# Kernel tuning notes

Hardware: AMD Instinct MI355X
Metric: run time of the kernel (lower is better)

Reference implementation:

```python
import jax, jax.numpy as jnp
import numpy as np

N_NODES = 50000
N_EDGES = 800000
H = 128
CHEM_DIM = 34   # 2 + 2*num_gdf
GEOM_DIM = 48   # 2*num_gdf + num_signatures
EPS = 1e-5


def _linear_params(key, d_in, d_out):
    kw, kb = jax.random.split(key)
    lim = 1.0 / np.sqrt(d_in)
    w = jax.random.uniform(kw, (d_in, d_out), jnp.float32, -lim, lim)
    b = jax.random.uniform(kb, (d_out,), jnp.float32, -lim, lim)
    return w, b


def setup_inputs() -> dict:
    key = jax.random.key(0)
    ks = jax.random.split(key, 16)
    inp = {
        'chem_feats': jax.random.normal(ks[0], (N_EDGES, CHEM_DIM), jnp.float32),
        'geom_feats': jax.random.normal(ks[1], (N_NODES, GEOM_DIM), jnp.float32),
        'nbr_vids': jax.random.randint(ks[2], (N_EDGES,), 0, N_NODES, jnp.int32),
    }
    # chem_mlp: Linear(34,128) -> BN(128) -> SiLU -> Linear(128,256) -> BN(256)
    inp['w_c1'], inp['b_c1'] = _linear_params(ks[3], CHEM_DIM, H)
    inp['g_c1'], inp['be_c1'] = jnp.ones((H,), jnp.float32), jnp.zeros((H,), jnp.float32)
    inp['w_c2'], inp['b_c2'] = _linear_params(ks[4], H, 2 * H)
    inp['g_c2'], inp['be_c2'] = jnp.ones((2 * H,), jnp.float32), jnp.zeros((2 * H,), jnp.float32)
    # geom_mlp: Linear(48,64) -> BN(64) -> SiLU -> Linear(64,64) -> BN(64)
    inp['w_g1'], inp['b_g1'] = _linear_params(ks[5], GEOM_DIM, H // 2)
    inp['g_g1'], inp['be_g1'] = jnp.ones((H // 2,), jnp.float32), jnp.zeros((H // 2,), jnp.float32)
    inp['w_g2'], inp['b_g2'] = _linear_params(ks[6], H // 2, H // 2)
    inp['g_g2'], inp['be_g2'] = jnp.ones((H // 2,), jnp.float32), jnp.zeros((H // 2,), jnp.float32)
    # feat_mlp: Linear(192,128) -> BN(128) -> SiLU -> Linear(128,128) -> BN(128)
    inp['w_f1'], inp['b_f1'] = _linear_params(ks[7], H + H // 2, H)
    inp['g_f1'], inp['be_f1'] = jnp.ones((H,), jnp.float32), jnp.zeros((H,), jnp.float32)
    inp['w_f2'], inp['b_f2'] = _linear_params(ks[8], H, H)
    inp['g_f2'], inp['be_f2'] = jnp.ones((H,), jnp.float32), jnp.zeros((H,), jnp.float32)
    return inp


def _bn(x, gamma, beta):
    # BatchNorm1d with batch statistics (training-mode normalization; dropout = identity at eval)
    m = jnp.mean(x, axis=0)
    v = jnp.var(x, axis=0)
    return gamma * (x - m) * jax.lax.rsqrt(v + EPS) + beta


def reference(chem_feats, geom_feats, nbr_vids,
              w_c1, b_c1, g_c1, be_c1, w_c2, b_c2, g_c2, be_c2,
              w_g1, b_g1, g_g1, be_g1, w_g2, b_g2, g_g2, be_g2,
              w_f1, b_f1, g_f1, be_f1, w_f2, b_f2, g_f2, be_f2):
    # chem branch: per-edge MLP
    h = _bn(chem_feats @ w_c1 + b_c1, g_c1, be_c1)
    h = jax.nn.silu(h)
    h = _bn(h @ w_c2 + b_c2, g_c2, be_c2)            # [E, 2H]
    nbr_filter, nbr_core = jnp.split(h, 2, axis=-1)
    h_chem = jax.nn.sigmoid(nbr_filter) * jax.nn.softplus(nbr_core)  # [E, H]
    # scatter-sum per-edge features into node bins
    h_chem = jax.ops.segment_sum(h_chem, nbr_vids, num_segments=N_NODES)  # [N, H]
    # geom branch: per-node MLP
    hg = _bn(geom_feats @ w_g1 + b_g1, g_g1, be_g1)
    hg = jax.nn.silu(hg)
    h_geom = _bn(hg @ w_g2 + b_g2, g_g2, be_g2)      # [N, H/2]
    # fuse
    hf = jnp.concatenate((h_chem, h_geom), axis=-1)  # [N, 3H/2]
    hf = _bn(hf @ w_f1 + b_f1, g_f1, be_f1)
    hf = jax.nn.silu(hf)
    h_out = _bn(hf @ w_f2 + b_f2, g_f2, be_f2)       # [N, H]
    return h_out
```

## Files before the change

### kernel.cpp

```cpp
#include <hip/hip_runtime.h>
#include <hip/hip_bf16.h>
#include <cmath>

#define E_EDGES 800000
#define N_NODES 50000
#define BN_EPS 1e-5f

typedef __attribute__((ext_vector_type(8))) short short8;
typedef __attribute__((ext_vector_type(4))) float float4v;
typedef __attribute__((ext_vector_type(4))) unsigned int uint4v;
typedef unsigned short ushort_t;

#define MFMA16(a, b, c) __builtin_amdgcn_mfma_f32_16x16x32_bf16((a), (b), (c), 0, 0, 0)

#define OFF_GX 0
#define OFF_GH 2304
#define OFF_A1 23040
#define OFF_C1 23168
#define OFF_A2 23296
#define OFF_C2 23552
#define OFF_GS1SUM 23808
#define OFF_GS1SQ 23872
#define OFF_GS2SUM 23936
#define OFF_GS2SQ 24000
#define OFF_FS1SUM 24064
#define OFF_FS1SQ 24192
#define OFF_FS2SUM 24320
#define OFF_FS2SQ 24448
#define OFF_NODE 24576
#define OFF_TG2 (OFF_NODE + N_NODES * 128)
#define OFF_TF1 (OFF_TG2 + N_NODES * 64)
#define OFF_TF2 OFF_NODE
#define OFF_W1T (OFF_TF1 + N_NODES * 128)
#define OFF_W2T (OFF_W1T + 4096)
#define OFF_BASEI (OFF_W2T + 16384)
#define OFF_BTOT (OFF_BASEI + 50176)
#define OFF_CNT (OFF_BTOT + 256)
#define OFF_CUR (OFF_CNT + 50176)
#define OFF_SIDX (OFF_CUR + 50176)
#define OFF_VIDS (OFF_SIDX + E_EDGES)

__device__ __forceinline__ float frcp_(float x) { return __builtin_amdgcn_rcpf(x); }
__device__ __forceinline__ float sigmoid_(float x) { return frcp_(1.0f + __expf(-x)); }
__device__ __forceinline__ float softplus_(float x) {
  return (x > 20.0f) ? x : __logf(1.0f + __expf(x));
}
__device__ __forceinline__ float silu_(float x) { return x * frcp_(1.0f + __expf(-x)); }

__device__ __forceinline__ ushort_t f2bf(float f) {
  __hip_bfloat16 h = __float2bfloat16(f);
  return *(ushort_t*)&h;
}
__device__ __forceinline__ float bf2f(ushort_t u) {
  return __uint_as_float(((unsigned)u) << 16);
}
__device__ __forceinline__ unsigned cvtpk(float lo, float hi) {
  unsigned r;
  asm("v_cvt_pk_bf16_f32 %0, %1, %2" : "=v"(r) : "v"(lo), "v"(hi));
  return r;
}

__device__ __forceinline__ void load_xfrag(const float* __restrict__ chem, int e, int qd,
                                           short8* x0, short8* x1) {
  const float* xe = chem + e * 34;
  float2 p0 = *(const float2*)(xe + 8 * qd);
  float2 p1 = *(const float2*)(xe + 8 * qd + 2);
  float2 p2 = *(const float2*)(xe + 8 * qd + 4);
  float2 p3 = *(const float2*)(xe + 8 * qd + 6);
  union { short8 s; uint4v u; } cv;
  cv.u[0] = cvtpk(p0.x, p0.y);
  cv.u[1] = cvtpk(p1.x, p1.y);
  cv.u[2] = cvtpk(p2.x, p2.y);
  cv.u[3] = cvtpk(p3.x, p3.y);
  *x0 = cv.s;
  union { short8 s; uint4v u; } cb;
  cb.u = (uint4v){0, 0, 0, 0};
  if (qd == 0) {
    float2 pt = *(const float2*)(xe + 32);
    cb.u[0] = cvtpk(pt.x, pt.y);
  }
  *x1 = cb.s;
}

__global__ __launch_bounds__(256) void k_prep(const float* __restrict__ w1,
                                              const float* __restrict__ w2,
                                              float* __restrict__ ws) {
  ushort_t* w1t = (ushort_t*)(ws + OFF_W1T);
  ushort_t* w2t = (ushort_t*)(ws + OFF_W2T);
  int idx = blockIdx.x * 256 + threadIdx.x;
  if (idx < 128 * 64) {
    int c = idx >> 6, k = idx & 63;
    float v = (k < 34) ? w1[k * 128 + c] : 0.0f;
    w1t[idx] = f2bf(v);
  }
  int j = idx - 128 * 64;
  if (j >= 0 && j < 256 * 128) {
    int c = j >> 7, k = j & 127;
    w2t[j] = f2bf(w2[k * 256 + c]);
  }
}

__global__ __launch_bounds__(256) void k_hist(const int* __restrict__ vids,
                                              float* __restrict__ ws) {
  const int e = blockIdx.x * 256 + threadIdx.x;
  int* cnt = (int*)(ws + OFF_CNT);
  if (e < E_EDGES) atomicAdd(&cnt[vids[e]], 1);
}

__global__ __launch_bounds__(256) void k_scan1(float* __restrict__ ws) {
  const int* cnt = (const int*)(ws + OFF_CNT);
  int* base = (int*)(ws + OFF_BASEI);
  int* btot = (int*)(ws + OFF_BTOT);
  const int t = threadIdx.x, b = blockIdx.x, i = b * 256 + t;
  const int lane = t & 63, w = t >> 6;
  int c = (i < N_NODES) ? cnt[i] : 0;
  int s = c;
#pragma unroll
  for (int o = 1; o < 64; o <<= 1) {
    int y = __shfl_up(s, o);
    if (lane >= o) s += y;
  }
  __shared__ int wsum[4];
  if (lane == 63) wsum[w] = s;
  __syncthreads();
  int add = 0;
#pragma unroll
  for (int k = 0; k < 4; ++k)
    if (k < w) add += wsum[k];
  base[i] = s + add - c;
  if (t == 255) btot[b] = s + add;
}

__global__ __launch_bounds__(256) void k_scan2(float* __restrict__ ws) {
  int* btot = (int*)(ws + OFF_BTOT);
  const int t = threadIdx.x;
  const int lane = t & 63, w = t >> 6;
  int c = (t < 196) ? btot[t] : 0;
  int s = c;
#pragma unroll
  for (int o = 1; o < 64; o <<= 1) {
    int y = __shfl_up(s, o);
    if (lane >= o) s += y;
  }
  __shared__ int wsum[4];
  if (lane == 63) wsum[w] = s;
  __syncthreads();
  int add = 0;
#pragma unroll
  for (int k = 0; k < 4; ++k)
    if (k < w) add += wsum[k];
  if (t < 196) btot[t] = s + add - c;
}

__global__ __launch_bounds__(256) void k_fill(const int* __restrict__ vids,
                                              float* __restrict__ ws) {
  const int e = blockIdx.x * 256 + threadIdx.x;
  const int* base = (const int*)(ws + OFF_BASEI);
  const int* btot = (const int*)(ws + OFF_BTOT);
  int* cur = (int*)(ws + OFF_CUR);
  int* sidx = (int*)(ws + OFF_SIDX);
  int* vsrt = (int*)(ws + OFF_VIDS);
  if (e < E_EDGES) {
    int v = vids[e];
    int pos = base[v] + btot[v >> 8] + atomicAdd(&cur[v], 1);
    sidx[pos] = e;
    vsrt[pos] = v;
  }
}

__global__ __launch_bounds__(256) void k_xstats(const float* __restrict__ chem,
                                                float* __restrict__ ws) {
  __shared__ __align__(16) ushort_t xT[2][48 * 72];
  const int t = threadIdx.x, wv = t >> 6, ln = t & 63, r15 = ln & 15, qd = ln >> 4;
  for (int i = t; i < 2 * 14 * 72; i += 256) {
    int b = i / (14 * 72), j = i % (14 * 72);
    int rr = j / 72, e = j % 72;
    xT[b][(34 + rr) * 72 + e] = (rr == 0 && e < 64) ? (ushort_t)0x3F80 : (ushort_t)0;
  }
  float4v g0 = {0, 0, 0, 0}, g1 = {0, 0, 0, 0};
#pragma unroll 2
  for (int it = 0; it < 10; ++it) {
    const int st = blockIdx.x * 10 + it;
    const int buf = it & 1;
    for (int i = t; i < 64 * 17; i += 256) {
      int e = i / 17, kp = i - e * 17;
      float2 v = *(const float2*)(chem + st * 2176 + e * 34 + 2 * kp);
      unsigned u = cvtpk(v.x, v.y);
      xT[buf][(2 * kp) * 72 + e] = (ushort_t)u;
      xT[buf][(2 * kp + 1) * 72 + e] = (ushort_t)(u >> 16);
    }
    __syncthreads();
    const ushort_t* xb = &xT[buf][0];
#pragma unroll
    for (int ks = 0; ks < 2; ++ks) {
      const ushort_t* xk = xb + ks * 32 + 8 * qd;
      short8 f0 = *(const short8*)&xk[(0 + r15) * 72];
      short8 f1 = *(const short8*)&xk[(16 + r15) * 72];
      short8 f2v = *(const short8*)&xk[(32 + r15) * 72];
      if (wv == 0) { g0 = MFMA16(f0, f0, g0); g1 = MFMA16(f0, f1, g1); }
      else if (wv == 1) { g0 = MFMA16(f0, f2v, g0); g1 = MFMA16(f1, f1, g1); }
      else if (wv == 2) { g0 = MFMA16(f1, f2v, g0); }
      else { g0 = MFMA16(f2v, f2v, g0); }
    }
  }
  float* GX = ws + OFF_GX;
  int ti0, tj0, ti1 = -1, tj1 = -1;
  if (wv == 0) { ti0 = 0; tj0 = 0; ti1 = 0; tj1 = 1; }
  else if (wv == 1) { ti0 = 0; tj0 = 2; ti1 = 1; tj1 = 1; }
  else if (wv == 2) { ti0 = 1; tj0 = 2; }
  else { ti0 = 2; tj0 = 2; }
#pragma unroll
  for (int r = 0; r < 4; ++r)
    atomicAdd(&GX[(16 * ti0 + 4 * qd + r) * 48 + 16 * tj0 + r15], g0[r]);
  if (ti1 >= 0)
#pragma unroll
    for (int r = 0; r < 4; ++r)
      atomicAdd(&GX[(16 * ti1 + 4 * qd + r) * 48 + 16 * tj1 + r15], g1[r]);
}

__global__ __launch_bounds__(64) void k_bn1(const float* __restrict__ b1,
                                            const float* __restrict__ g1,
                                            const float* __restrict__ be1,
                                            float* __restrict__ ws) {
  const int c = blockIdx.x, i = threadIdx.x;
  __shared__ float wc[34];
  const ushort_t* w1t = (const ushort_t*)(ws + OFF_W1T);
  const float* GX = ws + OFF_GX;
  if (i < 34) wc[i] = bf2f(w1t[c * 64 + i]);
  __syncthreads();
  float p = 0.0f, ps = 0.0f;
  if (i < 34) {
    float gi = 0.0f;
    for (int j = 0; j < 34; ++j) {
      int a = i, b = j;
      if ((a >> 4) > (b >> 4)) { int tt = a; a = b; b = tt; }
      gi += GX[a * 48 + b] * wc[j];
    }
    p = wc[i] * gi;
    ps = wc[i] * GX[i * 48 + 34];
  }
#pragma unroll
  for (int off = 1; off < 64; off <<= 1) {
    p += __shfl_xor(p, off);
    ps += __shfl_xor(ps, off);
  }
  if (i == 0) {
    const float E = (float)E_EDGES;
    float bc = b1[c];
    float sum = ps + E * bc;
    float sq = p + 2.0f * bc * ps + E * bc * bc;
    float m = sum / E, v = sq / E - m * m;
    float a = g1[c] * rsqrtf(v + BN_EPS);
    ws[OFF_A1 + c] = a;
    ws[OFF_C1 + c] = a * (bc - m) + be1[c];
  }
}

template <int TJA, int TJB>
__device__ __forceinline__ void ghstep(const ushort_t* hk, int r15, float4v (&g)[11]) {
  short8 f[TJB + 1];
#pragma unroll
  for (int i = 0; i <= TJB; ++i) f[i] = *(const short8*)&hk[(16 * i + r15) * 72];
  short8 f8 = *(const short8*)&hk[(128 + r15) * 72];
  int s = 0;
#pragma unroll
  for (int ti = 0; ti <= TJA; ++ti) { g[s] = MFMA16(f[ti], f[TJA], g[s]); ++s; }
  g[s] = MFMA16(f8, f[TJA], g[s]); ++s;
#pragma unroll
  for (int ti = 0; ti <= TJB; ++ti) { g[s] = MFMA16(f[ti], f[TJB], g[s]); ++s; }
  g[s] = MFMA16(f8, f[TJB], g[s]);
}

__device__ __forceinline__ void ghtile(float* GH, int ti, int tj, int r15, int qd,
                                       const float4v v) {
#pragma unroll
  for (int r = 0; r < 4; ++r)
    atomicAdd(&GH[(16 * ti + 4 * qd + r) * 144 + 16 * tj + r15], v[r]);
}

template <int TJA, int TJB>
__device__ __forceinline__ void ghflush(float* GH, int r15, int qd, const float4v (&g)[11]) {
  int s = 0;
#pragma unroll
  for (int ti = 0; ti <= TJA; ++ti) { ghtile(GH, ti, TJA, r15, qd, g[s]); ++s; }
  ghtile(GH, 8, TJA, r15, qd, g[s]); ++s;
#pragma unroll
  for (int ti = 0; ti <= TJB; ++ti) { ghtile(GH, ti, TJB, r15, qd, g[s]); ++s; }
  ghtile(GH, 8, TJB, r15, qd, g[s]);
}

__global__ __launch_bounds__(256) void k_h(const float* __restrict__ chem,
                                           float* __restrict__ ws) {
  __shared__ __align__(16) ushort_t hT[2][144 * 72];
  const int t = threadIdx.x, wv = t >> 6, ln = t & 63, r15 = ln & 15, qd = ln >> 4;
  const ushort_t* w1t = (const ushort_t*)(ws + OFF_W1T);
  for (int i = t; i < 2 * 16 * 72; i += 256) {
    int b = i / (16 * 72), j = i % (16 * 72);
    int rr = j / 72, e = j % 72;
    hT[b][(128 + rr) * 72 + e] = (rr == 0 && e < 64) ? (ushort_t)0x3F80 : (ushort_t)0;
  }
  float a1c[2], c1c[2];
#pragma unroll
  for (int cf = 0; cf < 2; ++cf) {
    int col = 32 * wv + 16 * cf + r15;
    a1c[cf] = ws[OFF_A1 + col];
    c1c[cf] = ws[OFF_C1 + col];
  }
  float4v gacc[11];
#pragma unroll
  for (int s = 0; s < 11; ++s) gacc[s] = (float4v){0, 0, 0, 0};

#pragma unroll 2
  for (int it = 0; it < 10; ++it) {
    const int st = blockIdx.x * 10 + it;
    const int buf = it & 1;
    const int e_base = st * 64;
    short8 xa0[4], xa1[4];
#pragma unroll
    for (int rb = 0; rb < 4; ++rb)
      load_xfrag(chem, e_base + 16 * rb + r15, qd, &xa0[rb], &xa1[rb]);
#pragma unroll
    for (int cf = 0; cf < 2; ++cf) {
      const int col = 32 * wv + 16 * cf + r15;
      short8 wb0 = *(const short8*)&w1t[col * 64 + 8 * qd];
      short8 wb1 = *(const short8*)&w1t[col * 64 + 32 + 8 * qd];
#pragma unroll
      for (int rb = 0; rb < 4; ++rb) {
        float4v acc = (float4v){0, 0, 0, 0};
        acc = MFMA16(xa0[rb], wb0, acc);
        acc = MFMA16(xa1[rb], wb1, acc);
        float h0 = silu_(fmaf(a1c[cf], acc[0], c1c[cf]));
        float h1 = silu_(fmaf(a1c[cf], acc[1], c1c[cf]));
        float h2 = silu_(fmaf(a1c[cf], acc[2], c1c[cf]));
        float h3 = silu_(fmaf(a1c[cf], acc[3], c1c[cf]));
        unsigned lo = cvtpk(h0, h1), hi = cvtpk(h2, h3);
        unsigned long long pk = ((unsigned long long)hi << 32) | (unsigned long long)lo;
        *(unsigned long long*)&hT[buf][col * 72 + 16 * rb + 4 * qd] = pk;
      }
    }
    __syncthreads();
    const ushort_t* hb = &hT[buf][0];
#pragma unroll
    for (int ks = 0; ks < 2; ++ks) {
      const ushort_t* hk = hb + ks * 32 + 8 * qd;
      if (wv == 0) ghstep<0, 7>(hk, r15, gacc);
      else if (wv == 1) ghstep<1, 6>(hk, r15, gacc);
      else if (wv == 2) ghstep<2, 5>(hk, r15, gacc);
      else ghstep<3, 4>(hk, r15, gacc);
    }
  }
  float* GH = ws + OFF_GH;
  if (wv == 0) ghflush<0, 7>(GH, r15, qd, gacc);
  else if (wv == 1) ghflush<1, 6>(GH, r15, qd, gacc);
  else if (wv == 2) ghflush<2, 5>(GH, r15, qd, gacc);
  else ghflush<3, 4>(GH, r15, qd, gacc);
}

__global__ __launch_bounds__(128) void k_bn2(const float* __restrict__ b2,
                                             const float* __restrict__ g2,
                                             const float* __restrict__ be2,
                                             float* __restrict__ ws) {
  const int c = blockIdx.x, i = threadIdx.x;
  __shared__ float wcol[128];
  __shared__ float redQ[2], redS[2];
  const ushort_t* w2t = (const ushort_t*)(ws + OFF_W2T);
  const float* GH = ws + OFF_GH;
  wcol[i] = bf2f(w2t[c * 128 + i]);
  __syncthreads();
  float wi = wcol[i];
  float gi = 0.0f;
  for (int j = 0; j < 128; ++j) {
    int a = i, b = j;
    if ((a >> 4) > (b >> 4)) { int tt = a; a = b; b = tt; }
    gi += GH[a * 144 + b] * wcol[j];
  }
  float p = wi * gi;
  float ps = wi * GH[128 * 144 + i];
#pragma unroll
  for (int off = 1; off < 64; off <<= 1) {
    p += __shfl_xor(p, off);
    ps += __shfl_xor(ps, off);
  }
  const int wv = i >> 6, ln = i & 63;
  if (ln == 0) { redQ[wv] = p; redS[wv] = ps; }
  __syncthreads();
  if (i == 0) {
    float q = redQ[0] + redQ[1], s = redS[0] + redS[1];
    const float E = (float)E_EDGES;
    float bc = b2[c];
    float sum = s + E * bc;
    float sq = q + 2.0f * bc * s + E * bc * bc;
    float m = sum / E, v = sq / E - m * m;
    float a = g2[c] * rsqrtf(v + BN_EPS);
    ws[OFF_A2 + c] = a;
    ws[OFF_C2 + c] = a * (bc - m) + be2[c];
  }
}

__global__ __launch_bounds__(256) void k_scatter(const float* __restrict__ chem,
                                                 float* __restrict__ ws) {
  __shared__ __align__(16) ushort_t hS[64 * 136];
  __shared__ __align__(16) float gS[32 * 133];
  __shared__ int vS[64];
  const int t = threadIdx.x, wv = t >> 6, ln = t & 63, r15 = ln & 15, qd = ln >> 4;
  const ushort_t* w1t = (const ushort_t*)(ws + OFF_W1T);
  const ushort_t* w2t = (const ushort_t*)(ws + OFF_W2T);
  const int* sidx = (const int*)(ws + OFF_SIDX);
  const int* vsrt = (const int*)(ws + OFF_VIDS);
  float* node = ws + OFF_NODE;
  float a1c[2], c1c[2], aF2[2], cF2[2], aC2[2], cC2[2];
#pragma unroll
  for (int cf = 0; cf < 2; ++cf) {
    int col = 32 * wv + 16 * cf + r15;
    a1c[cf] = ws[OFF_A1 + col];
    c1c[cf] = ws[OFF_C1 + col];
    aF2[cf] = ws[OFF_A2 + col];
    cF2[cf] = ws[OFF_C2 + col];
    aC2[cf] = ws[OFF_A2 + 128 + col];
    cC2[cf] = ws[OFF_C2 + 128 + col];
  }
  const int st0 = blockIdx.x * 8;
  int eid_cur = 0, vid_cur = 0;
  if (st0 < 12500) { eid_cur = sidx[st0 * 64 + ln]; vid_cur = vsrt[st0 * 64 + ln]; }
  for (int it = 0; it < 8; ++it) {
    const int st = st0 + it;
    if (st >= 12500) break;
    int eid_nxt = 0, vid_nxt = 0;
    if (it < 7 && st + 1 < 12500) {
      eid_nxt = sidx[(st + 1) * 64 + ln];
      vid_nxt = vsrt[(st + 1) * 64 + ln];
    }
    short8 xa0[4], xa1[4];
#pragma unroll
    for (int rb = 0; rb < 4; ++rb) {
      int er = __shfl(eid_cur, 16 * rb + r15);
      load_xfrag(chem, er, qd, &xa0[rb], &xa1[rb]);
    }
#pragma unroll
    for (int cf = 0; cf < 2; ++cf) {
      const int col = 32 * wv + 16 * cf + r15;
      short8 wb0 = *(const short8*)&w1t[col * 64 + 8 * qd];
      short8 wb1 = *(const short8*)&w1t[col * 64 + 32 + 8 * qd];
#pragma unroll
      for (int rb = 0; rb < 4; ++rb) {
        float4v acc = (float4v){0, 0, 0, 0};
        acc = MFMA16(xa0[rb], wb0, acc);
        acc = MFMA16(xa1[rb], wb1, acc);
#pragma unroll
        for (int r = 0; r < 4; ++r) {
          float hv = silu_(fmaf(a1c[cf], acc[r], c1c[cf]));
          hS[(16 * rb + 4 * qd + r) * 136 + col] = (ushort_t)cvtpk(hv, hv);
        }
      }
    }
    __syncthreads();
    if (t < 64) vS[t] = vid_cur;
#pragma unroll
    for (int ch = 0; ch < 2; ++ch) {
#pragma unroll
      for (int cf = 0; cf < 2; ++cf) {
        const int colF = 32 * wv + 16 * cf + r15;
        float4v accF[2], accC[2];
#pragma unroll
        for (int rbb = 0; rbb < 2; ++rbb) {
          accF[rbb] = (float4v){0, 0, 0, 0};
          accC[rbb] = (float4v){0, 0, 0, 0};
        }
#pragma unroll
        for (int ks = 0; ks < 4; ++ks) {
          short8 bF = *(const short8*)&w2t[colF * 128 + ks * 32 + 8 * qd];
          short8 bC = *(const short8*)&w2t[(128 + colF) * 128 + ks * 32 + 8 * qd];
#pragma unroll
          for (int rbb = 0; rbb < 2; ++rbb) {
            const int rb = 2 * ch + rbb;
            short8 hf = *(const short8*)&hS[(16 * rb + r15) * 136 + ks * 32 + 8 * qd];
            accF[rbb] = MFMA16(hf, bF, accF[rbb]);
            accC[rbb] = MFMA16(hf, bC, accC[rbb]);
          }
        }
#pragma unroll
        for (int rbb = 0; rbb < 2; ++rbb)
#pragma unroll
          for (int r = 0; r < 4; ++r) {
            float F = fmaf(aF2[cf], accF[rbb][r], cF2[cf]);
            float Co = fmaf(aC2[cf], accC[rbb][r], cC2[cf]);
            gS[(16 * rbb + 4 * qd + r) * 133 + colF] = sigmoid_(F) * softplus_(Co);
          }
      }
      __syncthreads();
      {
        const int c = t & 127, sub = t >> 7;
        const float* g = &gS[(16 * sub) * 133 + c];
        const int* vv = &vS[32 * ch + 16 * sub];
        float acc = g[0];
        int vcur = vv[0];
#pragma unroll
        for (int r = 1; r < 16; ++r) {
          int v = vv[r];
          float x = g[r * 133];
          if (v != vcur) {
            atomicAdd(node + (size_t)vcur * 128 + c, acc);
            acc = 0.0f;
            vcur = v;
          }
          acc += x;
        }
        atomicAdd(node + (size_t)vcur * 128 + c, acc);
      }
      __syncthreads();
    }
    eid_cur = eid_nxt;
    vid_cur = vid_nxt;
  }
}

__global__ __launch_bounds__(256) void k_geom_stats1(const float* __restrict__ geom,
                                                     const float* __restrict__ wg1,
                                                     const float* __restrict__ bg1,
                                                     float* __restrict__ ws) {
  __shared__ float ssum[64], ssq[64];
  const int t = threadIdx.x, lane = t & 63, w = t >> 6;
  if (t < 64) { ssum[t] = 0.0f; ssq[t] = 0.0f; }
  __syncthreads();
  const float bcol = bg1[lane];
  const int nb = blockIdx.x * 16 + w * 4;
  float x[4], acc[4];
#pragma unroll
  for (int u = 0; u < 4; u++) {
    x[u] = (lane < 48) ? geom[(nb + u) * 48 + lane] : 0.0f;
    acc[u] = bcol;
  }
#pragma unroll 16
  for (int k = 0; k < 48; k++) {
    float wvv = wg1[k * 64 + lane];
#pragma unroll
    for (int u = 0; u < 4; u++) acc[u] = fmaf(__shfl(x[u], k), wvv, acc[u]);
  }
  float bs = 0.0f, bq = 0.0f;
#pragma unroll
  for (int u = 0; u < 4; u++) { bs += acc[u]; bq += acc[u] * acc[u]; }
  atomicAdd(&ssum[lane], bs);
  atomicAdd(&ssq[lane], bq);
  __syncthreads();
  if (t < 64) {
    atomicAdd(ws + OFF_GS1SUM + t, ssum[t]);
    atomicAdd(ws + OFF_GS1SQ + t, ssq[t]);
  }
}

__global__ __launch_bounds__(256) void k_geom_main(
    const float* __restrict__ geom, const float* __restrict__ wg1,
    const float* __restrict__ bg1, const float* __restrict__ gg1,
    const float* __restrict__ beg1, const float* __restrict__ wg2,
    const float* __restrict__ bg2, float* __restrict__ ws) {
  __shared__ float ssum[64], ssq[64];
  const int t = threadIdx.x, lane = t & 63, w = t >> 6;
  if (t < 64) { ssum[t] = 0.0f; ssq[t] = 0.0f; }
  const float invN = 1.0f / (float)N_NODES;
  float s1 = ws[OFF_GS1SUM + lane], q1 = ws[OFF_GS1SQ + lane];
  float m1 = s1 * invN, v1 = q1 * invN - m1 * m1;
  float a1 = gg1[lane] * rsqrtf(v1 + BN_EPS);
  float c1 = beg1[lane] - a1 * m1;
  const float bcol = bg1[lane], b2col = bg2[lane];
  __syncthreads();
  const int nb = blockIdx.x * 16 + w * 4;
  float x[4], tg1[4], hg[4], acc[4];
#pragma unroll
  for (int u = 0; u < 4; u++) {
    x[u] = (lane < 48) ? geom[(nb + u) * 48 + lane] : 0.0f;
    tg1[u] = bcol;
  }
#pragma unroll 16
  for (int k = 0; k < 48; k++) {
    float wvv = wg1[k * 64 + lane];
#pragma unroll
    for (int u = 0; u < 4; u++) tg1[u] = fmaf(__shfl(x[u], k), wvv, tg1[u]);
  }
#pragma unroll
  for (int u = 0; u < 4; u++) {
    hg[u] = silu_(fmaf(a1, tg1[u], c1));
    acc[u] = b2col;
  }
#pragma unroll 16
  for (int k = 0; k < 64; k++) {
    float wvv = wg2[k * 64 + lane];
#pragma unroll
    for (int u = 0; u < 4; u++) acc[u] = fmaf(__shfl(hg[u], k), wvv, acc[u]);
  }
  float bs = 0.0f, bq = 0.0f;
#pragma unroll
  for (int u = 0; u < 4; u++) {
    ws[OFF_TG2 + (nb + u) * 64 + lane] = acc[u];
    bs += acc[u]; bq += acc[u] * acc[u];
  }
  atomicAdd(&ssum[lane], bs);
  atomicAdd(&ssq[lane], bq);
  __syncthreads();
  if (t < 64) {
    atomicAdd(ws + OFF_GS2SUM + t, ssum[t]);
    atomicAdd(ws + OFF_GS2SQ + t, ssq[t]);
  }
}

__global__ __launch_bounds__(256) void k_fuse1(const float* __restrict__ wf1,
                                               const float* __restrict__ bf1,
                                               const float* __restrict__ gg2,
                                               const float* __restrict__ beg2,
                                               float* __restrict__ ws) {
  __shared__ float ssum[128], ssq[128];
  const int t = threadIdx.x, lane = t & 63, w = t >> 6;
  if (t < 128) { ssum[t] = 0.0f; ssq[t] = 0.0f; }
  const float invN = 1.0f / (float)N_NODES;
  float s2 = ws[OFF_GS2SUM + lane], q2 = ws[OFF_GS2SQ + lane];
  float mg = s2 * invN, vg = q2 * invN - mg * mg;
  float ag = gg2[lane] * rsqrtf(vg + BN_EPS);
  float cg_ = beg2[lane] - ag * mg;
  const float bA = bf1[lane], bB = bf1[64 + lane];
  __syncthreads();
  const int nb = blockIdx.x * 16 + w * 4;
  float xa[4], xb[4], xg[4], acc1[4], acc2[4];
#pragma unroll
  for (int u = 0; u < 4; u++) {
    int n = nb + u;
    xa[u] = ws[OFF_NODE + n * 128 + lane];
    xb[u] = ws[OFF_NODE + n * 128 + 64 + lane];
    xg[u] = fmaf(ag, ws[OFF_TG2 + n * 64 + lane], cg_);
    acc1[u] = bA; acc2[u] = bB;
  }
#pragma unroll 16
  for (int k = 0; k < 64; k++) {
    float w1v = wf1[k * 128 + lane], w2v = wf1[k * 128 + 64 + lane];
#pragma unroll
    for (int u = 0; u < 4; u++) {
      float xk = __shfl(xa[u], k);
      acc1[u] = fmaf(xk, w1v, acc1[u]);
      acc2[u] = fmaf(xk, w2v, acc2[u]);
    }
  }
#pragma unroll 16
  for (int k = 0; k < 64; k++) {
    float w1v = wf1[(64 + k) * 128 + lane], w2v = wf1[(64 + k) * 128 + 64 + lane];
#pragma unroll
    for (int u = 0; u < 4; u++) {
      float xk = __shfl(xb[u], k);
      acc1[u] = fmaf(xk, w1v, acc1[u]);
      acc2[u] = fmaf(xk, w2v, acc2[u]);
    }
  }
#pragma unroll 16
  for (int k = 0; k < 64; k++) {
    float w1v = wf1[(128 + k) * 128 + lane], w2v = wf1[(128 + k) * 128 + 64 + lane];
#pragma unroll
    for (int u = 0; u < 4; u++) {
      float xk = __shfl(xg[u], k);
      acc1[u] = fmaf(xk, w1v, acc1[u]);
      acc2[u] = fmaf(xk, w2v, acc2[u]);
    }
  }
  float sA = 0, qA = 0, sB = 0, qB = 0;
#pragma unroll
  for (int u = 0; u < 4; u++) {
    int n = nb + u;
    ws[OFF_TF1 + n * 128 + lane] = acc1[u];
    ws[OFF_TF1 + n * 128 + 64 + lane] = acc2[u];
    sA += acc1[u]; qA += acc1[u] * acc1[u];
    sB += acc2[u]; qB += acc2[u] * acc2[u];
  }
  atomicAdd(&ssum[lane], sA); atomicAdd(&ssq[lane], qA);
  atomicAdd(&ssum[64 + lane], sB); atomicAdd(&ssq[64 + lane], qB);
  __syncthreads();
  if (t < 128) {
    atomicAdd(ws + OFF_FS1SUM + t, ssum[t]);
    atomicAdd(ws + OFF_FS1SQ + t, ssq[t]);
  }
}

__global__ __launch_bounds__(256) void k_fuse2(const float* __restrict__ wf2,
                                               const float* __restrict__ bf2,
                                               const float* __restrict__ gf1,
                                               const float* __restrict__ bef1,
                                               float* __restrict__ ws) {
  __shared__ float ssum[128], ssq[128];
  const int t = threadIdx.x, lane = t & 63, w = t >> 6;
  if (t < 128) { ssum[t] = 0.0f; ssq[t] = 0.0f; }
  const float invN = 1.0f / (float)N_NODES;
  float sA_ = ws[OFF_FS1SUM + lane], qA_ = ws[OFF_FS1SQ + lane];
  float mA = sA_ * invN, vA = qA_ * invN - mA * mA;
  float aA = gf1[lane] * rsqrtf(vA + BN_EPS);
  float cA = bef1[lane] - aA * mA;
  float sB_ = ws[OFF_FS1SUM + 64 + lane], qB_ = ws[OFF_FS1SQ + 64 + lane];
  float mB = sB_ * invN, vB = qB_ * invN - mB * mB;
  float aB = gf1[64 + lane] * rsqrtf(vB + BN_EPS);
  float cB = bef1[64 + lane] - aB * mB;
  const float b1c = bf2[lane], b2c = bf2[64 + lane];
  __syncthreads();
  const int nb = blockIdx.x * 16 + w * 4;
  float ha[4], hb[4], acc1[4], acc2[4];
#pragma unroll
  for (int u = 0; u < 4; u++) {
    int n = nb + u;
    ha[u] = silu_(fmaf(aA, ws[OFF_TF1 + n * 128 + lane], cA));
    hb[u] = silu_(fmaf(aB, ws[OFF_TF1 + n * 128 + 64 + lane], cB));
    acc1[u] = b1c; acc2[u] = b2c;
  }
#pragma unroll 16
  for (int k = 0; k < 64; k++) {
    float w1v = wf2[k * 128 + lane], w2v = wf2[k * 128 + 64 + lane];
#pragma unroll
    for (int u = 0; u < 4; u++) {
      float xk = __shfl(ha[u], k);
      acc1[u] = fmaf(xk, w1v, acc1[u]);
      acc2[u] = fmaf(xk, w2v, acc2[u]);
    }
  }
#pragma unroll 16
  for (int k = 0; k < 64; k++) {
    float w1v = wf2[(64 + k) * 128 + lane], w2v = wf2[(64 + k) * 128 + 64 + lane];
#pragma unroll
    for (int u = 0; u < 4; u++) {
      float xk = __shfl(hb[u], k);
      acc1[u] = fmaf(xk, w1v, acc1[u]);
      acc2[u] = fmaf(xk, w2v, acc2[u]);
    }
  }
  float sA = 0, qA = 0, sB = 0, qB = 0;
#pragma unroll
  for (int u = 0; u < 4; u++) {
    int n = nb + u;
    ws[OFF_TF2 + n * 128 + lane] = acc1[u];
    ws[OFF_TF2 + n * 128 + 64 + lane] = acc2[u];
    sA += acc1[u]; qA += acc1[u] * acc1[u];
    sB += acc2[u]; qB += acc2[u] * acc2[u];
  }
  atomicAdd(&ssum[lane], sA); atomicAdd(&ssq[lane], qA);
  atomicAdd(&ssum[64 + lane], sB); atomicAdd(&ssq[64 + lane], qB);
  __syncthreads();
  if (t < 128) {
    atomicAdd(ws + OFF_FS2SUM + t, ssum[t]);
    atomicAdd(ws + OFF_FS2SQ + t, ssq[t]);
  }
}

__global__ __launch_bounds__(256) void k_final(const float* __restrict__ gf2,
                                               const float* __restrict__ bef2,
                                               const float* __restrict__ ws,
                                               float* __restrict__ out) {
  const int idx = blockIdx.x * 256 + threadIdx.x;
  const int base = idx * 4;
  if (base >= N_NODES * 128) return;
  const float invN = 1.0f / (float)N_NODES;
  const int c0 = base & 127;
  float4 v = *(const float4*)(ws + OFF_TF2 + base);
  float vv[4] = {v.x, v.y, v.z, v.w}, r[4];
#pragma unroll
  for (int j = 0; j < 4; j++) {
    int c = c0 + j;
    float s = ws[OFF_FS2SUM + c], q = ws[OFF_FS2SQ + c];
    float m = s * invN, var = q * invN - m * m;
    float a = gf2[c] * rsqrtf(var + BN_EPS);
    r[j] = fmaf(a, vv[j] - m, bef2[c]);
  }
  *(float4*)(out + base) = make_float4(r[0], r[1], r[2], r[3]);
}

extern "C" void kernel_launch(void* const* d_in, const int* in_sizes, int n_in,
                              void* d_out, int out_size, void* d_ws, size_t ws_size,
                              hipStream_t stream) {
  const float* chem = (const float*)d_in[0];
  const float* geom = (const float*)d_in[1];
  const int* vids = (const int*)d_in[2];
  const float* w_c1 = (const float*)d_in[3];  const float* b_c1 = (const float*)d_in[4];
  const float* g_c1 = (const float*)d_in[5];  const float* be_c1 = (const float*)d_in[6];
  const float* w_c2 = (const float*)d_in[7];  const float* b_c2 = (const float*)d_in[8];
  const float* g_c2 = (const float*)d_in[9];  const float* be_c2 = (const float*)d_in[10];
  const float* w_g1 = (const float*)d_in[11]; const float* b_g1 = (const float*)d_in[12];
  const float* g_g1 = (const float*)d_in[13]; const float* be_g1 = (const float*)d_in[14];
  const float* w_g2 = (const float*)d_in[15]; const float* b_g2 = (const float*)d_in[16];
  const float* g_g2 = (const float*)d_in[17]; const float* be_g2 = (const float*)d_in[18];
  const float* w_f1 = (const float*)d_in[19]; const float* b_f1 = (const float*)d_in[20];
  const float* g_f1 = (const float*)d_in[21]; const float* be_f1 = (const float*)d_in[22];
  const float* w_f2 = (const float*)d_in[23]; const float* b_f2 = (const float*)d_in[24];
  const float* g_f2 = (const float*)d_in[25]; const float* be_f2 = (const float*)d_in[26];
  float* ws = (float*)d_ws;
  float* out = (float*)d_out;

  hipMemsetAsync(d_ws, 0, (size_t)(OFF_NODE + N_NODES * 128) * sizeof(float), stream);
  hipMemsetAsync((void*)(ws + OFF_CNT), 0, (size_t)(2 * 50176) * sizeof(int), stream);

  k_prep<<<dim3(160), dim3(256), 0, stream>>>(w_c1, w_c2, ws);
  k_hist<<<dim3(3125), dim3(256), 0, stream>>>(vids, ws);
  k_scan1<<<dim3(196), dim3(256), 0, stream>>>(ws);
  k_scan2<<<dim3(1), dim3(256), 0, stream>>>(ws);
  k_fill<<<dim3(3125), dim3(256), 0, stream>>>(vids, ws);
  k_xstats<<<dim3(1250), dim3(256), 0, stream>>>(chem, ws);
  k_bn1<<<dim3(128), dim3(64), 0, stream>>>(b_c1, g_c1, be_c1, ws);
  k_h<<<dim3(1250), dim3(256), 0, stream>>>(chem, ws);
  k_bn2<<<dim3(256), dim3(128), 0, stream>>>(b_c2, g_c2, be_c2, ws);
  k_scatter<<<dim3(1563), dim3(256), 0, stream>>>(chem, ws);
  k_geom_stats1<<<dim3(3125), dim3(256), 0, stream>>>(geom, w_g1, b_g1, ws);
  k_geom_main<<<dim3(3125), dim3(256), 0, stream>>>(geom, w_g1, b_g1, g_g1, be_g1, w_g2, b_g2, ws);
  k_fuse1<<<dim3(3125), dim3(256), 0, stream>>>(w_f1, b_f1, g_g2, be_g2, ws);
  k_fuse2<<<dim3(3125), dim3(256), 0, stream>>>(w_f2, b_f2, g_f1, be_f1, ws);
  k_final<<<dim3(6250), dim3(256), 0, stream>>>(g_f2, be_f2, ws, out);
}
```

Measured before the change: 1.283 ms.

## Materialize first-layer hidden activations in k_h and reuse them in scatter

k_h now writes the bf16 SiLU hidden layer for every edge to a workspace buffer when the workspace is large enough. The scatter kernel then gathers those rows into LDS with direct global-to-LDS loads (XOR-swizzled) instead of reloading chem features and recomputing the first linear layer. It also processes all 64 edges per step in one pass with a larger gS. The goal is to remove the duplicated first-layer MFMA work, at the cost of about 200 MB of extra write and gather traffic, and it relies on ws_size being large enough, otherwise the fallback runs.

```diff
diff --git a/kernel.cpp b/kernel.cpp
--- a/kernel.cpp
+++ b/kernel.cpp
@@ -39,6 +39,7 @@
 #define OFF_CUR (OFF_CNT + 50176)
 #define OFF_SIDX (OFF_CUR + 50176)
 #define OFF_VIDS (OFF_SIDX + E_EDGES)
+#define OFF_HLIN (OFF_VIDS + E_EDGES)
 
 __device__ __forceinline__ float frcp_(float x) { return __builtin_amdgcn_rcpf(x); }
 __device__ __forceinline__ float sigmoid_(float x) { return frcp_(1.0f + __expf(-x)); }
@@ -58,6 +59,11 @@
   unsigned r;
   asm("v_cvt_pk_bf16_f32 %0, %1, %2" : "=v"(r) : "v"(lo), "v"(hi));
   return r;
+}
+__device__ __forceinline__ void gload_lds16(const void* g, void* l) {
+  __builtin_amdgcn_global_load_lds(
+      (const __attribute__((address_space(1))) unsigned int*)g,
+      (__attribute__((address_space(3))) unsigned int*)l, 16, 0, 0);
 }
 
 __device__ __forceinline__ void load_xfrag(const float* __restrict__ chem, int e, int qd,
@@ -290,7 +296,7 @@
 }
 
 __global__ __launch_bounds__(256) void k_h(const float* __restrict__ chem,
-                                           float* __restrict__ ws) {
+                                           float* __restrict__ ws, int store_h) {
   __shared__ __align__(16) ushort_t hT[2][144 * 72];
   const int t = threadIdx.x, wv = t >> 6, ln = t & 63, r15 = ln & 15, qd = ln >> 4;
   const ushort_t* w1t = (const ushort_t*)(ws + OFF_W1T);
@@ -339,6 +345,24 @@
       }
     }
     __syncthreads();
+    if (store_h) {
+      unsigned* hlin = (unsigned*)(ws + OFF_HLIN);
+      const int e_loc = t >> 2, qq = t & 3;
+      const ushort_t* hb2 = &hT[buf][0];
+      unsigned* dst = hlin + (size_t)(e_base + e_loc) * 64 + 16 * qq;
+#pragma unroll
+      for (int jj = 0; jj < 4; ++jj) {
+        uint4v o;
+#pragma unroll
+        for (int m = 0; m < 4; ++m) {
+          int u = 16 * qq + 4 * jj + m;
+          unsigned lo = hb2[(2 * u) * 72 + e_loc];
+          unsigned hi = hb2[(2 * u + 1) * 72 + e_loc];
+          o[m] = lo | (hi << 16);
+        }
+        *(uint4v*)(dst + 4 * jj) = o;
+      }
+    }
     const ushort_t* hb = &hT[buf][0];
 #pragma unroll
     for (int ks = 0; ks < 2; ++ks) {
@@ -397,23 +421,20 @@
   }
 }
 
-__global__ __launch_bounds__(256) void k_scatter(const float* __restrict__ chem,
-                                                 float* __restrict__ ws) {
-  __shared__ __align__(16) ushort_t hS[64 * 136];
-  __shared__ __align__(16) float gS[32 * 133];
+__global__ __launch_bounds__(256) void k_scatter(float* __restrict__ ws) {
+  __shared__ __align__(16) ushort_t hS[64 * 128];
+  __shared__ __align__(16) float gS[64 * 133];
   __shared__ int vS[64];
   const int t = threadIdx.x, wv = t >> 6, ln = t & 63, r15 = ln & 15, qd = ln >> 4;
-  const ushort_t* w1t = (const ushort_t*)(ws + OFF_W1T);
   const ushort_t* w2t = (const ushort_t*)(ws + OFF_W2T);
   const int* sidx = (const int*)(ws + OFF_SIDX);
   const int* vsrt = (const int*)(ws + OFF_VIDS);
+  const unsigned* hlin = (const unsigned*)(ws + OFF_HLIN);
   float* node = ws + OFF_NODE;
-  float a1c[2], c1c[2], aF2[2], cF2[2], aC2[2], cC2[2];
+  float aF2[2], cF2[2], aC2[2], cC2[2];
 #pragma unroll
   for (int cf = 0; cf < 2; ++cf) {
     int col = 32 * wv + 16 * cf + r15;
-    a1c[cf] = ws[OFF_A1 + col];
-    c1c[cf] = ws[OFF_C1 + col];
     aF2[cf] = ws[OFF_A2 + col];
     cF2[cf] = ws[OFF_C2 + col];
     aC2[cf] = ws[OFF_A2 + 128 + col];
@@ -430,10 +451,106 @@
       eid_nxt = sidx[(st + 1) * 64 + ln];
       vid_nxt = vsrt[(st + 1) * 64 + ln];
     }
+#pragma unroll
+    for (int k = 0; k < 4; ++k) {
+      const int row = 16 * wv + 4 * k + qd;
+      const int er = __shfl(eid_cur, row);
+      const int c = (ln & 15) ^ (row & 15);
+      gload_lds16(hlin + (size_t)er * 64 + 4 * c, (void*)&hS[(16 * wv + 4 * k) * 128]);
+    }
+    __syncthreads();
+    if (t < 64) vS[t] = vid_cur;
+    short8 hf[4][4];
+#pragma unroll
+    for (int ks = 0; ks < 4; ++ks)
+#pragma unroll
+      for (int rb = 0; rb < 4; ++rb)
+        hf[ks][rb] = *(const short8*)&hS[(16 * rb + r15) * 128 + ((4 * ks + qd) ^ r15) * 8];
+#pragma unroll
+    for (int cf = 0; cf < 2; ++cf) {
+      const int colF = 32 * wv + 16 * cf + r15;
+      float4v accF[4], accC[4];
+#pragma unroll
+      for (int rb = 0; rb < 4; ++rb) {
+        accF[rb] = (float4v){0, 0, 0, 0};
+        accC[rb] = (float4v){0, 0, 0, 0};
+      }
+#pragma unroll
+      for (int ks = 0; ks < 4; ++ks) {
+        short8 bF = *(const short8*)&w2t[colF * 128 + ks * 32 + 8 * qd];
+        short8 bC = *(const short8*)&w2t[(128 + colF) * 128 + ks * 32 + 8 * qd];
+#pragma unroll
+        for (int rb = 0; rb < 4; ++rb) {
+          accF[rb] = MFMA16(hf[ks][rb], bF, accF[rb]);
+          accC[rb] = MFMA16(hf[ks][rb], bC, accC[rb]);
+        }
+      }
+#pragma unroll
+      for (int rb = 0; rb < 4; ++rb)
+#pragma unroll
+        for (int r = 0; r < 4; ++r) {
+          float F = fmaf(aF2[cf], accF[rb][r], cF2[cf]);
+          float Co = fmaf(aC2[cf], accC[rb][r], cC2[cf]);
+          gS[(16 * rb + 4 * qd + r) * 133 + colF] = sigmoid_(F) * softplus_(Co);
+        }
+    }
+    __syncthreads();
+    {
+      const int c = t & 127, half = t >> 7;
+      const float* g = &gS[(32 * half) * 133 + c];
+      const int* vv = &vS[32 * half];
+      float acc = g[0];
+      int vcur = vv[0];
+#pragma unroll
+      for (int r = 1; r < 32; ++r) {
+        int v = vv[r];
+        float x = g[r * 133];
+        if (v != vcur) {
+          atomicAdd(node + (size_t)vcur * 128 + c, acc);
+          acc = 0.0f;
+          vcur = v;
+        }
+        acc += x;
+      }
+      atomicAdd(node + (size_t)vcur * 128 + c, acc);
+    }
+    eid_cur = eid_nxt;
+    vid_cur = vid_nxt;
+  }
+}
+
+__global__ __launch_bounds__(256) void k_scatter_fb(const float* __restrict__ chem,
+                                                    float* __restrict__ ws) {
+  __shared__ __align__(16) ushort_t hS[64 * 136];
+  __shared__ __align__(16) float gS[64 * 133];
+  __shared__ int vS[64];
+  const int t = threadIdx.x, wv = t >> 6, ln = t & 63, r15 = ln & 15, qd = ln >> 4;
+  const ushort_t* w1t = (const ushort_t*)(ws + OFF_W1T);
+  const ushort_t* w2t = (const ushort_t*)(ws + OFF_W2T);
+  const int* sidx = (const int*)(ws + OFF_SIDX);
+  const int* vsrt = (const int*)(ws + OFF_VIDS);
+  float* node = ws + OFF_NODE;
+  float a1c[2], c1c[2], aF2[2], cF2[2], aC2[2], cC2[2];
+#pragma unroll
+  for (int cf = 0; cf < 2; ++cf) {
+    int col = 32 * wv + 16 * cf + r15;
+    a1c[cf] = ws[OFF_A1 + col];
+    c1c[cf] = ws[OFF_C1 + col];
+    aF2[cf] = ws[OFF_A2 + col];
+    cF2[cf] = ws[OFF_C2 + col];
+    aC2[cf] = ws[OFF_A2 + 128 + col];
+    cC2[cf] = ws[OFF_C2 + 128 + col];
+  }
+  for (int it = 0; it < 8; ++it) {
+    const int st = blockIdx.x * 8 + it;
+    if (st >= 12500) break;
+    const int e_base = st * 64;
+    const int myeid = sidx[e_base + ln];
+    const int myvid = vsrt[e_base + ln];
     short8 xa0[4], xa1[4];
 #pragma unroll
     for (int rb = 0; rb < 4; ++rb) {
-      int er = __shfl(eid_cur, 16 * rb + r15);
+      int er = __shfl(myeid, 16 * rb + r15);
       load_xfrag(chem, er, qd, &xa0[rb], &xa1[rb]);
     }
 #pragma unroll
@@ -454,63 +571,56 @@
       }
     }
     __syncthreads();
-    if (t < 64) vS[t] = vid_cur;
-#pragma unroll
-    for (int ch = 0; ch < 2; ++ch) {
-#pragma unroll
-      for (int cf = 0; cf < 2; ++cf) {
-        const int colF = 32 * wv + 16 * cf + r15;
-        float4v accF[2], accC[2];
-#pragma unroll
-        for (int rbb = 0; rbb < 2; ++rbb) {
-          accF[rbb] = (float4v){0, 0, 0, 0};
-          accC[rbb] = (float4v){0, 0, 0, 0};
+    if (t < 64) vS[t] = myvid;
+#pragma unroll
+    for (int cf = 0; cf < 2; ++cf) {
+      const int colF = 32 * wv + 16 * cf + r15;
+      float4v accF[4], accC[4];
+#pragma unroll
+      for (int rb = 0; rb < 4; ++rb) {
+        accF[rb] = (float4v){0, 0, 0, 0};
+        accC[rb] = (float4v){0, 0, 0, 0};
+      }
+#pragma unroll
+      for (int ks = 0; ks < 4; ++ks) {
+        short8 bF = *(const short8*)&w2t[colF * 128 + ks * 32 + 8 * qd];
+        short8 bC = *(const short8*)&w2t[(128 + colF) * 128 + ks * 32 + 8 * qd];
+#pragma unroll
+        for (int rb = 0; rb < 4; ++rb) {
+          short8 hf = *(const short8*)&hS[(16 * rb + r15) * 136 + ks * 32 + 8 * qd];
+          accF[rb] = MFMA16(hf, bF, accF[rb]);
+          accC[rb] = MFMA16(hf, bC, accC[rb]);
         }
-#pragma unroll
-        for (int ks = 0; ks < 4; ++ks) {
-          short8 bF = *(const short8*)&w2t[colF * 128 + ks * 32 + 8 * qd];
-          short8 bC = *(const short8*)&w2t[(128 + colF) * 128 + ks * 32 + 8 * qd];
-#pragma unroll
-          for (int rbb = 0; rbb < 2; ++rbb) {
-            const int rb = 2 * ch + rbb;
-            short8 hf = *(const short8*)&hS[(16 * rb + r15) * 136 + ks * 32 + 8 * qd];
-            accF[rbb] = MFMA16(hf, bF, accF[rbb]);
-            accC[rbb] = MFMA16(hf, bC, accC[rbb]);
-          }
+      }
+#pragma unroll
+      for (int rb = 0; rb < 4; ++rb)
+#pragma unroll
+        for (int r = 0; r < 4; ++r) {
+          float F = fmaf(aF2[cf], accF[rb][r], cF2[cf]);
+          float Co = fmaf(aC2[cf], accC[rb][r], cC2[cf]);
+          gS[(16 * rb + 4 * qd + r) * 133 + colF] = sigmoid_(F) * softplus_(Co);
         }
-#pragma unroll
-        for (int rbb = 0; rbb < 2; ++rbb)
-#pragma unroll
-          for (int r = 0; r < 4; ++r) {
-            float F = fmaf(aF2[cf], accF[rbb][r], cF2[cf]);
-            float Co = fmaf(aC2[cf], accC[rbb][r], cC2[cf]);
-            gS[(16 * rbb + 4 * qd + r) * 133 + colF] = sigmoid_(F) * softplus_(Co);
-          }
+    }
+    __syncthreads();
+    {
+      const int c = t & 127, half = t >> 7;
+      const float* g = &gS[(32 * half) * 133 + c];
+      const int* vv = &vS[32 * half];
+      float acc = g[0];
+      int vcur = vv[0];
+#pragma unroll
+      for (int r = 1; r < 32; ++r) {
+        int v = vv[r];
+        float x = g[r * 133];
+        if (v != vcur) {
+          atomicAdd(node + (size_t)vcur * 128 + c, acc);
+          acc = 0.0f;
+          vcur = v;
+        }
+        acc += x;
       }
-      __syncthreads();
-      {
-        const int c = t & 127, sub = t >> 7;
-        const float* g = &gS[(16 * sub) * 133 + c];
-        const int* vv = &vS[32 * ch + 16 * sub];
-        float acc = g[0];
-        int vcur = vv[0];
-#pragma unroll
-        for (int r = 1; r < 16; ++r) {
-          int v = vv[r];
-          float x = g[r * 133];
-          if (v != vcur) {
-            atomicAdd(node + (size_t)vcur * 128 + c, acc);
-            acc = 0.0f;
-            vcur = v;
-          }
-          acc += x;
-        }
-        atomicAdd(node + (size_t)vcur * 128 + c, acc);
-      }
-      __syncthreads();
-    }
-    eid_cur = eid_nxt;
-    vid_cur = vid_nxt;
+      atomicAdd(node + (size_t)vcur * 128 + c, acc);
+    }
   }
 }
 
@@ -784,6 +894,9 @@
   float* ws = (float*)d_ws;
   float* out = (float*)d_out;
 
+  const size_t need_ws = ((size_t)OFF_HLIN + (size_t)E_EDGES * 64) * sizeof(float);
+  const int big = (ws_size >= need_ws) ? 1 : 0;
+
   hipMemsetAsync(d_ws, 0, (size_t)(OFF_NODE + N_NODES * 128) * sizeof(float), stream);
   hipMemsetAsync((void*)(ws + OFF_CNT), 0, (size_t)(2 * 50176) * sizeof(int), stream);
 
@@ -794,9 +907,10 @@
   k_fill<<<dim3(3125), dim3(256), 0, stream>>>(vids, ws);
   k_xstats<<<dim3(1250), dim3(256), 0, stream>>>(chem, ws);
   k_bn1<<<dim3(128), dim3(64), 0, stream>>>(b_c1, g_c1, be_c1, ws);
-  k_h<<<dim3(1250), dim3(256), 0, stream>>>(chem, ws);
+  k_h<<<dim3(1250), dim3(256), 0, stream>>>(chem, ws, big);
   k_bn2<<<dim3(256), dim3(128), 0, stream>>>(b_c2, g_c2, be_c2, ws);
-  k_scatter<<<dim3(1563), dim3(256), 0, stream>>>(chem, ws);
+  if (big) k_scatter<<<dim3(1563), dim3(256), 0, stream>>>(ws);
+  else     k_scatter_fb<<<dim3(1563), dim3(256), 0, stream>>>(chem, ws);
   k_geom_stats1<<<dim3(3125), dim3(256), 0, stream>>>(geom, w_g1, b_g1, ws);
   k_geom_main<<<dim3(3125), dim3(256), 0, stream>>>(geom, w_g1, b_g1, g_g1, be_g1, w_g2, b_g2, ws);
   k_fuse1<<<dim3(3125), dim3(256), 0, stream>>>(w_f1, b_f1, g_g2, be_g2, ws);
```

Measured after the change: 1.233 ms. -3.9%, faster.

## Fuse histogram into xstats and software-pipeline scatter kernel gathers

Applied to the files above, without the earlier changes.

Folds the per-node edge-count histogram into the k_xstats kernel, which removes one launch. In k_scatter, the next tile's chem rows are prefetched into registers while the current tile computes. The second GEMM now processes all 64 rows in one pass with a larger shared gS buffer, cutting four __syncthreads to two lighter LDS-only barriers per tile. The costs are higher register pressure (hinted to 3 waves via launch bounds) and more LDS per block.

```diff
diff --git a/kernel.cpp b/kernel.cpp
--- a/kernel.cpp
+++ b/kernel.cpp
@@ -59,6 +59,11 @@
   asm("v_cvt_pk_bf16_f32 %0, %1, %2" : "=v"(r) : "v"(lo), "v"(hi));
   return r;
 }
+__device__ __forceinline__ void lds_barrier() {
+  asm volatile("s_waitcnt lgkmcnt(0)" ::: "memory");
+  __builtin_amdgcn_s_barrier();
+  asm volatile("" ::: "memory");
+}
 
 __device__ __forceinline__ void load_xfrag(const float* __restrict__ chem, int e, int qd,
                                            short8* x0, short8* x1) {
@@ -100,13 +105,6 @@
   }
 }
 
-__global__ __launch_bounds__(256) void k_hist(const int* __restrict__ vids,
-                                              float* __restrict__ ws) {
-  const int e = blockIdx.x * 256 + threadIdx.x;
-  int* cnt = (int*)(ws + OFF_CNT);
-  if (e < E_EDGES) atomicAdd(&cnt[vids[e]], 1);
-}
-
 __global__ __launch_bounds__(256) void k_scan1(float* __restrict__ ws) {
   const int* cnt = (const int*)(ws + OFF_CNT);
   int* base = (int*)(ws + OFF_BASEI);
@@ -169,9 +167,15 @@
 }
 
 __global__ __launch_bounds__(256) void k_xstats(const float* __restrict__ chem,
+                                                const int* __restrict__ vids,
                                                 float* __restrict__ ws) {
   __shared__ __align__(16) ushort_t xT[2][48 * 72];
   const int t = threadIdx.x, wv = t >> 6, ln = t & 63, r15 = ln & 15, qd = ln >> 4;
+  {
+    int* cnt = (int*)(ws + OFF_CNT);
+    const int e0 = blockIdx.x * 640;
+    for (int i = t; i < 640; i += 256) atomicAdd(&cnt[vids[e0 + i]], 1);
+  }
   for (int i = t; i < 2 * 14 * 72; i += 256) {
     int b = i / (14 * 72), j = i % (14 * 72);
     int rr = j / 72, e = j % 72;
@@ -397,10 +401,10 @@
   }
 }
 
-__global__ __launch_bounds__(256) void k_scatter(const float* __restrict__ chem,
-                                                 float* __restrict__ ws) {
+__global__ __launch_bounds__(256, 3) void k_scatter(const float* __restrict__ chem,
+                                                    float* __restrict__ ws) {
   __shared__ __align__(16) ushort_t hS[64 * 136];
-  __shared__ __align__(16) float gS[32 * 133];
+  __shared__ __align__(16) float gS[64 * 133];
   __shared__ int vS[64];
   const int t = threadIdx.x, wv = t >> 6, ln = t & 63, r15 = ln & 15, qd = ln >> 4;
   const ushort_t* w1t = (const ushort_t*)(ws + OFF_W1T);
@@ -420,21 +424,57 @@
     cC2[cf] = ws[OFF_C2 + 128 + col];
   }
   const int st0 = blockIdx.x * 8;
-  int eid_cur = 0, vid_cur = 0;
-  if (st0 < 12500) { eid_cur = sidx[st0 * 64 + ln]; vid_cur = vsrt[st0 * 64 + ln]; }
-  for (int it = 0; it < 8; ++it) {
-    const int st = st0 + it;
-    if (st >= 12500) break;
-    int eid_nxt = 0, vid_nxt = 0;
-    if (it < 7 && st + 1 < 12500) {
-      eid_nxt = sidx[(st + 1) * 64 + ln];
-      vid_nxt = vsrt[(st + 1) * 64 + ln];
-    }
+  const int nt = (12500 - st0 < 8) ? (12500 - st0) : 8;
+  int eid_c = sidx[st0 * 64 + ln], vid_c = vsrt[st0 * 64 + ln];
+  float2 xp[4][4], xt[4];
+#pragma unroll
+  for (int rb = 0; rb < 4; ++rb) xt[rb] = make_float2(0.0f, 0.0f);
+#pragma unroll
+  for (int rb = 0; rb < 4; ++rb) {
+    int er = __shfl(eid_c, 16 * rb + r15);
+    const float* xe = chem + er * 34 + 8 * qd;
+    xp[rb][0] = *(const float2*)(xe);
+    xp[rb][1] = *(const float2*)(xe + 2);
+    xp[rb][2] = *(const float2*)(xe + 4);
+    xp[rb][3] = *(const float2*)(xe + 6);
+    if (qd == 0) xt[rb] = *(const float2*)(chem + er * 34 + 32);
+  }
+  int eid_n = 0, vid_n = 0;
+  if (nt > 1) {
+    eid_n = sidx[(st0 + 1) * 64 + ln];
+    vid_n = vsrt[(st0 + 1) * 64 + ln];
+  }
+  for (int it = 0; it < nt; ++it) {
     short8 xa0[4], xa1[4];
 #pragma unroll
     for (int rb = 0; rb < 4; ++rb) {
-      int er = __shfl(eid_cur, 16 * rb + r15);
-      load_xfrag(chem, er, qd, &xa0[rb], &xa1[rb]);
+      union { short8 s; uint4v u; } cv;
+      cv.u[0] = cvtpk(xp[rb][0].x, xp[rb][0].y);
+      cv.u[1] = cvtpk(xp[rb][1].x, xp[rb][1].y);
+      cv.u[2] = cvtpk(xp[rb][2].x, xp[rb][2].y);
+      cv.u[3] = cvtpk(xp[rb][3].x, xp[rb][3].y);
+      xa0[rb] = cv.s;
+      union { short8 s; uint4v u; } cb;
+      cb.u = (uint4v){0, 0, 0, 0};
+      if (qd == 0) cb.u[0] = cvtpk(xt[rb].x, xt[rb].y);
+      xa1[rb] = cb.s;
+    }
+    if (it + 1 < nt) {
+#pragma unroll
+      for (int rb = 0; rb < 4; ++rb) {
+        int er = __shfl(eid_n, 16 * rb + r15);
+        const float* xe = chem + er * 34 + 8 * qd;
+        xp[rb][0] = *(const float2*)(xe);
+        xp[rb][1] = *(const float2*)(xe + 2);
+        xp[rb][2] = *(const float2*)(xe + 4);
+        xp[rb][3] = *(const float2*)(xe + 6);
+        if (qd == 0) xt[rb] = *(const float2*)(chem + er * 34 + 32);
+      }
+    }
+    int eid_n2 = 0, vid_n2 = 0;
+    if (it + 2 < nt) {
+      eid_n2 = sidx[(st0 + it + 2) * 64 + ln];
+      vid_n2 = vsrt[(st0 + it + 2) * 64 + ln];
     }
 #pragma unroll
     for (int cf = 0; cf < 2; ++cf) {
@@ -453,64 +493,64 @@
         }
       }
     }
-    __syncthreads();
-    if (t < 64) vS[t] = vid_cur;
-#pragma unroll
-    for (int ch = 0; ch < 2; ++ch) {
-#pragma unroll
-      for (int cf = 0; cf < 2; ++cf) {
-        const int colF = 32 * wv + 16 * cf + r15;
-        float4v accF[2], accC[2];
-#pragma unroll
-        for (int rbb = 0; rbb < 2; ++rbb) {
-          accF[rbb] = (float4v){0, 0, 0, 0};
-          accC[rbb] = (float4v){0, 0, 0, 0};
+    lds_barrier();
+    if (t < 64) vS[t] = vid_c;
+    short8 hf[4][4];
+#pragma unroll
+    for (int ks = 0; ks < 4; ++ks)
+#pragma unroll
+      for (int rb = 0; rb < 4; ++rb)
+        hf[ks][rb] = *(const short8*)&hS[(16 * rb + r15) * 136 + ks * 32 + 8 * qd];
+#pragma unroll
+    for (int cf = 0; cf < 2; ++cf) {
+      const int colF = 32 * wv + 16 * cf + r15;
+      float4v accF[4], accC[4];
+#pragma unroll
+      for (int rb = 0; rb < 4; ++rb) {
+        accF[rb] = (float4v){0, 0, 0, 0};
+        accC[rb] = (float4v){0, 0, 0, 0};
+      }
+#pragma unroll
+      for (int ks = 0; ks < 4; ++ks) {
+        short8 bF = *(const short8*)&w2t[colF * 128 + ks * 32 + 8 * qd];
+        short8 bC = *(const short8*)&w2t[(128 + colF) * 128 + ks * 32 + 8 * qd];
+#pragma unroll
+        for (int rb = 0; rb < 4; ++rb) {
+          accF[rb] = MFMA16(hf[ks][rb], bF, accF[rb]);
+          accC[rb] = MFMA16(hf[ks][rb], bC, accC[rb]);
         }
-#pragma unroll
-        for (int ks = 0; ks < 4; ++ks) {
-          short8 bF = *(const short8*)&w2t[colF * 128 + ks * 32 + 8 * qd];
-          short8 bC = *(const short8*)&w2t[(128 + colF) * 128 + ks * 32 + 8 * qd];
-#pragma unroll
-          for (int rbb = 0; rbb < 2; ++rbb) {
-            const int rb = 2 * ch + rbb;
-            short8 hf = *(const short8*)&hS[(16 * rb + r15) * 136 + ks * 32 + 8 * qd];
-            accF[rbb] = MFMA16(hf, bF, accF[rbb]);
-            accC[rbb] = MFMA16(hf, bC, accC[rbb]);
-          }
+      }
+#pragma unroll
+      for (int rb = 0; rb < 4; ++rb)
+#pragma unroll
+        for (int r = 0; r < 4; ++r) {
+          float F = fmaf(aF2[cf], accF[rb][r], cF2[cf]);
+          float Co = fmaf(aC2[cf], accC[rb][r], cC2[cf]);
+          gS[(16 * rb + 4 * qd + r) * 133 + colF] = sigmoid_(F) * softplus_(Co);
         }
-#pragma unroll
-        for (int rbb = 0; rbb < 2; ++rbb)
-#pragma unroll
-          for (int r = 0; r < 4; ++r) {
-            float F = fmaf(aF2[cf], accF[rbb][r], cF2[cf]);
-            float Co = fmaf(aC2[cf], accC[rbb][r], cC2[cf]);
-            gS[(16 * rbb + 4 * qd + r) * 133 + colF] = sigmoid_(F) * softplus_(Co);
-          }
+    }
+    lds_barrier();
+    {
+      const int c = t & 127, half = t >> 7;
+      const float* g = &gS[(32 * half) * 133 + c];
+      const int* vv = &vS[32 * half];
+      float acc = g[0];
+      int vcur = vv[0];
+#pragma unroll
+      for (int r = 1; r < 32; ++r) {
+        int v = vv[r];
+        float x = g[r * 133];
+        if (v != vcur) {
+          atomicAdd(node + (size_t)vcur * 128 + c, acc);
+          acc = 0.0f;
+          vcur = v;
+        }
+        acc += x;
       }
-      __syncthreads();
-      {
-        const int c = t & 127, sub = t >> 7;
-        const float* g = &gS[(16 * sub) * 133 + c];
-        const int* vv = &vS[32 * ch + 16 * sub];
-        float acc = g[0];
-        int vcur = vv[0];
-#pragma unroll
-        for (int r = 1; r < 16; ++r) {
-          int v = vv[r];
-          float x = g[r * 133];
-          if (v != vcur) {
-            atomicAdd(node + (size_t)vcur * 128 + c, acc);
-            acc = 0.0f;
-            vcur = v;
-          }
-          acc += x;
-        }
-        atomicAdd(node + (size_t)vcur * 128 + c, acc);
-      }
-      __syncthreads();
-    }
-    eid_cur = eid_nxt;
-    vid_cur = vid_nxt;
+      atomicAdd(node + (size_t)vcur * 128 + c, acc);
+    }
+    eid_c = eid_n; vid_c = vid_n;
+    eid_n = eid_n2; vid_n = vid_n2;
   }
 }
 
@@ -788,11 +828,10 @@
   hipMemsetAsync((void*)(ws + OFF_CNT), 0, (size_t)(2 * 50176) * sizeof(int), stream);
 
   k_prep<<<dim3(160), dim3(256), 0, stream>>>(w_c1, w_c2, ws);
-  k_hist<<<dim3(3125), dim3(256), 0, stream>>>(vids, ws);
+  k_xstats<<<dim3(1250), dim3(256), 0, stream>>>(chem, vids, ws);
   k_scan1<<<dim3(196), dim3(256), 0, stream>>>(ws);
   k_scan2<<<dim3(1), dim3(256), 0, stream>>>(ws);
   k_fill<<<dim3(3125), dim3(256), 0, stream>>>(vids, ws);
-  k_xstats<<<dim3(1250), dim3(256), 0, stream>>>(chem, ws);
   k_bn1<<<dim3(128), dim3(64), 0, stream>>>(b_c1, g_c1, be_c1, ws);
   k_h<<<dim3(1250), dim3(256), 0, stream>>>(chem, ws);
   k_bn2<<<dim3(256), dim3(128), 0, stream>>>(b_c2, g_c2, be_c2, ws);
```

Result: faster. 1.253 ms (-2.3%).
